# Performance work log

Hardware: AMD Instinct MI355X
Metric: run time of the kernel (lower is better)

## Reference

```python
import jax, jax.numpy as jnp
import numpy as np

D_ENC, D_DEC, HID = 512, 512, 256

def setup_inputs() -> dict:
    key = jax.random.key(0)
    ks = jax.random.split(key, 8)
    B, T, U = 4, 800, 150
    enc = jax.random.normal(ks[0], (B, T, D_ENC), dtype=jnp.float32)
    dec = jax.random.normal(ks[1], (B, U, D_DEC), dtype=jnp.float32)
    s_e = 1.0 / np.sqrt(D_ENC)
    s_d = 1.0 / np.sqrt(D_DEC)
    s_h = 1.0 / np.sqrt(HID)
    W_enc = jax.random.uniform(ks[2], (D_ENC, HID), jnp.float32, -s_e, s_e)
    b_enc = jax.random.uniform(ks[3], (HID,), jnp.float32, -s_e, s_e)
    W_dec = jax.random.uniform(ks[4], (D_DEC, HID), jnp.float32, -s_d, s_d)
    b_dec = jax.random.uniform(ks[5], (HID,), jnp.float32, -s_d, s_d)
    w_score = jax.random.uniform(ks[6], (HID,), jnp.float32, -s_h, s_h)
    b_score = jax.random.uniform(ks[7], (), jnp.float32, -s_h, s_h)
    return {"encoder_out": enc, "decoder_out": dec,
            "W_enc": W_enc, "b_enc": b_enc,
            "W_dec": W_dec, "b_dec": b_dec,
            "w_score": w_score, "b_score": b_score}

def reference(encoder_out, decoder_out, W_enc, b_enc, W_dec, b_dec, w_score, b_score):
    # enc_proj: [B,T,H], dec_proj: [B,U,H]
    enc_proj = jnp.einsum('bte,eh->bth', encoder_out, W_enc) + b_enc
    dec_proj = jnp.einsum('bud,dh->buh', decoder_out, W_dec) + b_dec
    # Broadcast-add + tanh -> [B,T,U,H], then reduce H with score vector.
    combined = jnp.tanh(enc_proj[:, :, None, :] + dec_proj[:, None, :, :])
    score = jnp.einsum('btuh,h->btu', combined, w_score) + b_score
    # Softmax over decoder tokens (last dim U).
    return jax.nn.softmax(score, axis=-1)
```

## Files before the change

kernel.cpp:

```cpp
#include <hip/hip_runtime.h>
#include <hip/hip_bf16.h>

#define B_ 4
#define T_ 800
#define U_ 150
#define D_ 512
#define H_ 256
#define PADH2 132

static constexpr float ARG_SCALE = 2.8853900817779268f;
static constexpr float LOG2E_F   = 1.4426950408889634f;

extern "C" __device__ float __ocml_exp2_f32(float);

__device__ __forceinline__ float fast_exp2(float x) {
#if __has_builtin(__builtin_amdgcn_exp2f)
    return __builtin_amdgcn_exp2f(x);
#else
    return __ocml_exp2_f32(x);
#endif
}
__device__ __forceinline__ float fast_rcp(float x) {
#if __has_builtin(__builtin_amdgcn_rcpf)
    return __builtin_amdgcn_rcpf(x);
#else
    return 1.0f / x;
#endif
}

__device__ __forceinline__ float4 fma4(float4 w, float x, float4 a) {
    a.x = fmaf(w.x, x, a.x); a.y = fmaf(w.y, x, a.y);
    a.z = fmaf(w.z, x, a.z); a.w = fmaf(w.w, x, a.w);
    return a;
}

__global__ __launch_bounds__(256) void proj_exp_kernel(
    const float* __restrict__ enc, const float* __restrict__ dec,
    const float* __restrict__ W_enc, const float* __restrict__ b_enc,
    const float* __restrict__ W_dec, const float* __restrict__ b_dec,
    float* __restrict__ Ee, float* __restrict__ Ed)
{
    const int tid = threadIdx.x;
    const int blk = blockIdx.x;
    const float* in; const float* Wm; const float* bias; float* outp; int row0;
    if (blk < 400) { in = enc; Wm = W_enc; bias = b_enc; outp = Ee; row0 = blk * 8; }
    else           { in = dec; Wm = W_dec; bias = b_dec; outp = Ed; row0 = (blk - 400) * 8; }

    const int h4  = tid & 63;
    const int wid = __builtin_amdgcn_readfirstlane(tid >> 6);
    const int eq  = wid * 128;

    const float* wp = Wm + (size_t)eq * H_ + 4 * h4;
    const float* ip0 = in + (size_t)(row0 + 0) * D_ + eq;
    const float* ip1 = in + (size_t)(row0 + 1) * D_ + eq;
    const float* ip2 = in + (size_t)(row0 + 2) * D_ + eq;
    const float* ip3 = in + (size_t)(row0 + 3) * D_ + eq;
    const float* ip4 = in + (size_t)(row0 + 4) * D_ + eq;
    const float* ip5 = in + (size_t)(row0 + 5) * D_ + eq;
    const float* ip6 = in + (size_t)(row0 + 6) * D_ + eq;
    const float* ip7 = in + (size_t)(row0 + 7) * D_ + eq;

    float4 acc[8] = {};
    #pragma unroll 2
    for (int e = 0; e < 128; e += 4) {
        float4 w0 = *(const float4*)(wp + (size_t)(e + 0) * H_);
        float4 w1 = *(const float4*)(wp + (size_t)(e + 1) * H_);
        float4 w2 = *(const float4*)(wp + (size_t)(e + 2) * H_);
        float4 w3 = *(const float4*)(wp + (size_t)(e + 3) * H_);
        float4 x0 = *(const float4*)(ip0 + e);
        float4 x1 = *(const float4*)(ip1 + e);
        float4 x2 = *(const float4*)(ip2 + e);
        float4 x3 = *(const float4*)(ip3 + e);
        float4 x4 = *(const float4*)(ip4 + e);
        float4 x5 = *(const float4*)(ip5 + e);
        float4 x6 = *(const float4*)(ip6 + e);
        float4 x7 = *(const float4*)(ip7 + e);
        acc[0] = fma4(w3, x0.w, fma4(w2, x0.z, fma4(w1, x0.y, fma4(w0, x0.x, acc[0]))));
        acc[1] = fma4(w3, x1.w, fma4(w2, x1.z, fma4(w1, x1.y, fma4(w0, x1.x, acc[1]))));
        acc[2] = fma4(w3, x2.w, fma4(w2, x2.z, fma4(w1, x2.y, fma4(w0, x2.x, acc[2]))));
        acc[3] = fma4(w3, x3.w, fma4(w2, x3.z, fma4(w1, x3.y, fma4(w0, x3.x, acc[3]))));
        acc[4] = fma4(w3, x4.w, fma4(w2, x4.z, fma4(w1, x4.y, fma4(w0, x4.x, acc[4]))));
        acc[5] = fma4(w3, x5.w, fma4(w2, x5.z, fma4(w1, x5.y, fma4(w0, x5.x, acc[5]))));
        acc[6] = fma4(w3, x6.w, fma4(w2, x6.z, fma4(w1, x6.y, fma4(w0, x6.x, acc[6]))));
        acc[7] = fma4(w3, x7.w, fma4(w2, x7.z, fma4(w1, x7.y, fma4(w0, x7.x, acc[7]))));
    }

    __shared__ float red[4][8][H_];
    #pragma unroll
    for (int r = 0; r < 8; ++r)
        *(float4*)&red[wid][r][4 * h4] = acc[r];
    __syncthreads();

    const int rr = tid >> 5;
    const int hq = tid & 31;
    #pragma unroll
    for (int s = 0; s < 2; ++s) {
        const int hp = hq + 32 * s;
        float4 a0 = *(const float4*)&red[0][rr][4 * hp];
        float4 a1 = *(const float4*)&red[1][rr][4 * hp];
        float4 a2 = *(const float4*)&red[2][rr][4 * hp];
        float4 a3 = *(const float4*)&red[3][rr][4 * hp];
        float4 b4 = *(const float4*)(bias + 4 * hp);
        float4 v;
        v.x = fast_exp2(ARG_SCALE * (((a0.x + a1.x) + (a2.x + a3.x)) + b4.x));
        v.y = fast_exp2(ARG_SCALE * (((a0.y + a1.y) + (a2.y + a3.y)) + b4.y));
        v.z = fast_exp2(ARG_SCALE * (((a0.z + a1.z) + (a2.z + a3.z)) + b4.z));
        v.w = fast_exp2(ARG_SCALE * (((a0.w + a1.w) + (a2.w + a3.w)) + b4.w));
        *(float4*)(outp + (size_t)(row0 + rr) * H_ + 4 * hp) = v;
    }
}

__global__ __launch_bounds__(128) void score_kernel(
    const float* __restrict__ Ee, const float* __restrict__ Ed,
    const float* __restrict__ w_score,
    float* __restrict__ sc0, float* __restrict__ sc1)
{
    const int tid = threadIdx.x;
    const int ut = blockIdx.x % 5, hs = blockIdx.x / 5;
    const int tt = blockIdx.y, b = blockIdx.z;

    __shared__ float eld[32][PADH2];
    __shared__ float dld[32][PADH2];

    const int t0 = tt * 32, u0 = ut * 32;
    const int hoff = hs * 128;

    #pragma unroll
    for (int k = 0; k < 8; ++k) {
        int idx = tid + 128 * k;
        int row = idx >> 5;
        int f4  = idx & 31;
        *(float4*)&eld[row][4 * f4] =
            *(const float4*)(Ee + (size_t)(b * T_ + t0 + row) * H_ + hoff + 4 * f4);
        int du = u0 + row; if (du > U_ - 1) du = U_ - 1;
        *(float4*)&dld[row][4 * f4] =
            *(const float4*)(Ed + (size_t)(b * U_ + du) * H_ + hoff + 4 * f4);
    }
    __syncthreads();

    const int tx = tid & 15, ty = tid >> 4;
    const float* e0 = &eld[4 * ty + 0][0];
    const float* e1 = &eld[4 * ty + 1][0];
    const float* e2 = &eld[4 * ty + 2][0];
    const float* e3 = &eld[4 * ty + 3][0];
    const float* d0 = &dld[tx][0];
    const float* d1 = &dld[tx + 16][0];
    const float* wp = w_score + hoff;

    float4 z4 = {0.f, 0.f, 0.f, 0.f};
    float4 a00 = z4, a01 = z4, a10 = z4, a11 = z4;
    float4 a20 = z4, a21 = z4, a30 = z4, a31 = z4;

#define SIG(E, D) fast_rcp(fmaf((E), (D), 1.f))
#define ROW(A, EV, DV) \
    A.x = fmaf(w.x, SIG(EV.x, DV.x), A.x); \
    A.y = fmaf(w.y, SIG(EV.y, DV.y), A.y); \
    A.z = fmaf(w.z, SIG(EV.z, DV.z), A.z); \
    A.w = fmaf(w.w, SIG(EV.w, DV.w), A.w);

    #pragma unroll 4
    for (int h4 = 0; h4 < 32; ++h4) {
        float4 w  = ((const float4*)wp)[h4];
        float4 ea = *(const float4*)(e0 + 4 * h4);
        float4 eb = *(const float4*)(e1 + 4 * h4);
        float4 ec = *(const float4*)(e2 + 4 * h4);
        float4 ed = *(const float4*)(e3 + 4 * h4);
        float4 da = *(const float4*)(d0 + 4 * h4);
        float4 db = *(const float4*)(d1 + 4 * h4);
        ROW(a00, ea, da) ROW(a01, ea, db)
        ROW(a10, eb, da) ROW(a11, eb, db)
        ROW(a20, ec, da) ROW(a21, ec, db)
        ROW(a30, ed, da) ROW(a31, ed, db)
    }
#undef ROW
#undef SIG

    float s0[4], s1[4];
    s0[0] = (a00.x + a00.y) + (a00.z + a00.w);
    s0[1] = (a10.x + a10.y) + (a10.z + a10.w);
    s0[2] = (a20.x + a20.y) + (a20.z + a20.w);
    s0[3] = (a30.x + a30.y) + (a30.z + a30.w);
    s1[0] = (a01.x + a01.y) + (a01.z + a01.w);
    s1[1] = (a11.x + a11.y) + (a11.z + a11.w);
    s1[2] = (a21.x + a21.y) + (a21.z + a21.w);
    s1[3] = (a31.x + a31.y) + (a31.z + a31.w);

    float* sout = hs ? sc1 : sc0;
    const int ua = u0 + tx, ub = ua + 16;
    #pragma unroll
    for (int j = 0; j < 4; ++j) {
        const int t = t0 + 4 * ty + j;
        const size_t base = (size_t)(b * T_ + t) * U_;
        sout[base + ua] = s0[j];
        if (ub < U_) sout[base + ub] = s1[j];
    }
}

__global__ __launch_bounds__(256) void softmax_kernel(
    const float* __restrict__ sc0, const float* __restrict__ sc1,
    float* __restrict__ out)
{
    const int tid  = threadIdx.x;
    const int wave = tid >> 6, lane = tid & 63;
    const int row  = blockIdx.x * 4 + wave;
    const size_t base = (size_t)row * U_;

    float z0 = -2.f * (sc0[base + lane]      + sc1[base + lane]);
    float z1 = -2.f * (sc0[base + lane + 64] + sc1[base + lane + 64]);
    const bool v2 = (lane + 128) < U_;
    float z2 = v2 ? -2.f * (sc0[base + lane + 128] + sc1[base + lane + 128])
                  : -INFINITY;

    float m = fmaxf(fmaxf(z0, z1), z2);
    #pragma unroll
    for (int off = 32; off > 0; off >>= 1) m = fmaxf(m, __shfl_xor(m, off));

    float p0 = fast_exp2((z0 - m) * LOG2E_F);
    float p1 = fast_exp2((z1 - m) * LOG2E_F);
    float p2 = v2 ? fast_exp2((z2 - m) * LOG2E_F) : 0.f;

    float s = p0 + p1 + p2;
    #pragma unroll
    for (int off = 32; off > 0; off >>= 1) s += __shfl_xor(s, off);

    const float inv = 1.0f / s;
    out[base + lane]      = p0 * inv;
    out[base + lane + 64] = p1 * inv;
    if (v2) out[base + lane + 128] = p2 * inv;
}

extern "C" void kernel_launch(void* const* d_in, const int* in_sizes, int n_in,
                              void* d_out, int out_size, void* d_ws, size_t ws_size,
                              hipStream_t stream) {
    const float* enc     = (const float*)d_in[0];
    const float* dec     = (const float*)d_in[1];
    const float* W_enc   = (const float*)d_in[2];
    const float* b_enc   = (const float*)d_in[3];
    const float* W_dec   = (const float*)d_in[4];
    const float* b_dec   = (const float*)d_in[5];
    const float* w_score = (const float*)d_in[6];

    float* ws = (float*)d_ws;
    float* Ee  = ws;
    float* Ed  = Ee + 819200;
    float* sc0 = Ed + 153600;
    float* sc1 = sc0 + 480000;
    float* out = (float*)d_out;

    proj_exp_kernel<<<475, 256, 0, stream>>>(enc, dec, W_enc, b_enc, W_dec, b_dec, Ee, Ed);
    score_kernel<<<dim3(10, 25, 4), 128, 0, stream>>>(Ee, Ed, w_score, sc0, sc1);
    softmax_kernel<<<800, 256, 0, stream>>>(sc0, sc1, out);
}
```

Before: 44.46 us.

## Move projection GEMMs to bf16x3 split MFMA with pre-swizzled weights

Replaces the FP32 FMA projection kernel with an MFMA kernel. It splits each fp32 value into bf16 hi and lo parts and uses three bf16 MFMAs to keep near-fp32 accuracy. A new per-call kernel converts and re-lays out the weights into the MFMA B-fragment order, and activations are staged through swizzled LDS. This targets the scalar-FMA cost of the projections, at the price of an extra kernel launch, the conversion traffic and a small loss of precision.

```diff
diff --git a/kernel.cpp b/kernel.cpp
--- a/kernel.cpp
+++ b/kernel.cpp
@@ -11,6 +11,9 @@
 static constexpr float ARG_SCALE = 2.8853900817779268f;
 static constexpr float LOG2E_F   = 1.4426950408889634f;
 
+typedef __attribute__((ext_vector_type(8))) short bf16x8;
+typedef __attribute__((ext_vector_type(4))) float f32x4;
+
 extern "C" __device__ float __ocml_exp2_f32(float);
 
 __device__ __forceinline__ float fast_exp2(float x) {
@@ -28,85 +31,114 @@
 #endif
 }
 
-__device__ __forceinline__ float4 fma4(float4 w, float x, float4 a) {
-    a.x = fmaf(w.x, x, a.x); a.y = fmaf(w.y, x, a.y);
-    a.z = fmaf(w.z, x, a.z); a.w = fmaf(w.w, x, a.w);
-    return a;
-}
-
-__global__ __launch_bounds__(256) void proj_exp_kernel(
+__device__ __forceinline__ void bf16split(float x, unsigned short& hi, unsigned short& lo) {
+    unsigned u = __builtin_bit_cast(unsigned, x);
+    unsigned r = (u + 0x7FFFu + ((u >> 16) & 1u)) >> 16;
+    hi = (unsigned short)r;
+    float fh = __builtin_bit_cast(float, r << 16);
+    float d = x - fh;
+    unsigned u2 = __builtin_bit_cast(unsigned, d);
+    unsigned r2 = (u2 + 0x7FFFu + ((u2 >> 16) & 1u)) >> 16;
+    lo = (unsigned short)r2;
+}
+
+__global__ __launch_bounds__(256) void wconv_kernel(
+    const float* __restrict__ We, const float* __restrict__ Wd,
+    unsigned short* __restrict__ WtEh, unsigned short* __restrict__ WtEl,
+    unsigned short* __restrict__ WtDh, unsigned short* __restrict__ WtDl)
+{
+    const int blk = blockIdx.x;
+    const float* W; unsigned short *oh, *ol; int e;
+    if (blk < 512) { W = We; oh = WtEh; ol = WtEl; e = blk; }
+    else           { W = Wd; oh = WtDh; ol = WtDl; e = blk - 512; }
+    const int h = threadIdx.x;
+    float x = W[(size_t)e * H_ + h];
+    unsigned short hi, lo; bf16split(x, hi, lo);
+    const int s = e >> 5, q = (e >> 3) & 3, j = e & 7;
+    const int g = h >> 4, r = h & 15, l = q * 16 + r;
+    const size_t idx = (size_t)(s * 16 + g) * 512 + l * 8 + j;
+    oh[idx] = hi; ol[idx] = lo;
+}
+
+__global__ __launch_bounds__(256) void proj_mfma_kernel(
     const float* __restrict__ enc, const float* __restrict__ dec,
-    const float* __restrict__ W_enc, const float* __restrict__ b_enc,
-    const float* __restrict__ W_dec, const float* __restrict__ b_dec,
+    const unsigned short* __restrict__ WtEh, const unsigned short* __restrict__ WtEl,
+    const unsigned short* __restrict__ WtDh, const unsigned short* __restrict__ WtDl,
+    const float* __restrict__ b_enc, const float* __restrict__ b_dec,
     float* __restrict__ Ee, float* __restrict__ Ed)
 {
     const int tid = threadIdx.x;
-    const int blk = blockIdx.x;
-    const float* in; const float* Wm; const float* bias; float* outp; int row0;
-    if (blk < 400) { in = enc; Wm = W_enc; bias = b_enc; outp = Ee; row0 = blk * 8; }
-    else           { in = dec; Wm = W_dec; bias = b_dec; outp = Ed; row0 = (blk - 400) * 8; }
-
-    const int h4  = tid & 63;
-    const int wid = __builtin_amdgcn_readfirstlane(tid >> 6);
-    const int eq  = wid * 128;
-
-    const float* wp = Wm + (size_t)eq * H_ + 4 * h4;
-    const float* ip0 = in + (size_t)(row0 + 0) * D_ + eq;
-    const float* ip1 = in + (size_t)(row0 + 1) * D_ + eq;
-    const float* ip2 = in + (size_t)(row0 + 2) * D_ + eq;
-    const float* ip3 = in + (size_t)(row0 + 3) * D_ + eq;
-    const float* ip4 = in + (size_t)(row0 + 4) * D_ + eq;
-    const float* ip5 = in + (size_t)(row0 + 5) * D_ + eq;
-    const float* ip6 = in + (size_t)(row0 + 6) * D_ + eq;
-    const float* ip7 = in + (size_t)(row0 + 7) * D_ + eq;
-
-    float4 acc[8] = {};
-    #pragma unroll 2
-    for (int e = 0; e < 128; e += 4) {
-        float4 w0 = *(const float4*)(wp + (size_t)(e + 0) * H_);
-        float4 w1 = *(const float4*)(wp + (size_t)(e + 1) * H_);
-        float4 w2 = *(const float4*)(wp + (size_t)(e + 2) * H_);
-        float4 w3 = *(const float4*)(wp + (size_t)(e + 3) * H_);
-        float4 x0 = *(const float4*)(ip0 + e);
-        float4 x1 = *(const float4*)(ip1 + e);
-        float4 x2 = *(const float4*)(ip2 + e);
-        float4 x3 = *(const float4*)(ip3 + e);
-        float4 x4 = *(const float4*)(ip4 + e);
-        float4 x5 = *(const float4*)(ip5 + e);
-        float4 x6 = *(const float4*)(ip6 + e);
-        float4 x7 = *(const float4*)(ip7 + e);
-        acc[0] = fma4(w3, x0.w, fma4(w2, x0.z, fma4(w1, x0.y, fma4(w0, x0.x, acc[0]))));
-        acc[1] = fma4(w3, x1.w, fma4(w2, x1.z, fma4(w1, x1.y, fma4(w0, x1.x, acc[1]))));
-        acc[2] = fma4(w3, x2.w, fma4(w2, x2.z, fma4(w1, x2.y, fma4(w0, x2.x, acc[2]))));
-        acc[3] = fma4(w3, x3.w, fma4(w2, x3.z, fma4(w1, x3.y, fma4(w0, x3.x, acc[3]))));
-        acc[4] = fma4(w3, x4.w, fma4(w2, x4.z, fma4(w1, x4.y, fma4(w0, x4.x, acc[4]))));
-        acc[5] = fma4(w3, x5.w, fma4(w2, x5.z, fma4(w1, x5.y, fma4(w0, x5.x, acc[5]))));
-        acc[6] = fma4(w3, x6.w, fma4(w2, x6.z, fma4(w1, x6.y, fma4(w0, x6.x, acc[6]))));
-        acc[7] = fma4(w3, x7.w, fma4(w2, x7.z, fma4(w1, x7.y, fma4(w0, x7.x, acc[7]))));
-    }
-
-    __shared__ float red[4][8][H_];
-    #pragma unroll
-    for (int r = 0; r < 8; ++r)
-        *(float4*)&red[wid][r][4 * h4] = acc[r];
+    int blk = blockIdx.x;
+    const float* in; const unsigned short *Wh, *Wl; const float* bias; float* outp;
+    int rmax;
+    if (blk < 400) { in = enc; Wh = WtEh; Wl = WtEl; bias = b_enc; outp = Ee; rmax = B_ * T_ - 1; }
+    else { blk -= 400; in = dec; Wh = WtDh; Wl = WtDl; bias = b_dec; outp = Ed; rmax = B_ * U_ - 1; }
+    const int hh   = blk & 1;
+    const int row0 = (blk >> 1) * 16;
+
+    __shared__ unsigned short Ah[16 * 512];
+    __shared__ unsigned short Al[16 * 512];
+
+    #pragma unroll
+    for (int k = 0; k < 4; ++k) {
+        const int chunk = tid + 256 * k;
+        const int r = chunk >> 6;
+        const int c = chunk & 63;
+        int gr = row0 + r; if (gr > rmax) gr = rmax;
+        const float* src = in + (size_t)gr * D_ + c * 8;
+        const float4 f0 = ((const float4*)src)[0];
+        const float4 f1 = ((const float4*)src)[1];
+        float v[8] = {f0.x, f0.y, f0.z, f0.w, f1.x, f1.y, f1.z, f1.w};
+        bf16x8 ah, al;
+        #pragma unroll
+        for (int j = 0; j < 8; ++j) {
+            unsigned short hi, lo; bf16split(v[j], hi, lo);
+            ah[j] = (short)hi; al[j] = (short)lo;
+        }
+        const int di = r * 512 + ((c ^ (r & 7)) << 3);
+        *(bf16x8*)&Ah[di] = ah;
+        *(bf16x8*)&Al[di] = al;
+    }
     __syncthreads();
 
-    const int rr = tid >> 5;
-    const int hq = tid & 31;
-    #pragma unroll
-    for (int s = 0; s < 2; ++s) {
-        const int hp = hq + 32 * s;
-        float4 a0 = *(const float4*)&red[0][rr][4 * hp];
-        float4 a1 = *(const float4*)&red[1][rr][4 * hp];
-        float4 a2 = *(const float4*)&red[2][rr][4 * hp];
-        float4 a3 = *(const float4*)&red[3][rr][4 * hp];
-        float4 b4 = *(const float4*)(bias + 4 * hp);
-        float4 v;
-        v.x = fast_exp2(ARG_SCALE * (((a0.x + a1.x) + (a2.x + a3.x)) + b4.x));
-        v.y = fast_exp2(ARG_SCALE * (((a0.y + a1.y) + (a2.y + a3.y)) + b4.y));
-        v.z = fast_exp2(ARG_SCALE * (((a0.z + a1.z) + (a2.z + a3.z)) + b4.z));
-        v.w = fast_exp2(ARG_SCALE * (((a0.w + a1.w) + (a2.w + a3.w)) + b4.w));
-        *(float4*)(outp + (size_t)(row0 + rr) * H_ + 4 * hp) = v;
+    const int lane = tid & 63, w = tid >> 6;
+    const int q = lane >> 4, r15 = lane & 15;
+
+    f32x4 acc0 = {0.f, 0.f, 0.f, 0.f};
+    f32x4 acc1 = {0.f, 0.f, 0.f, 0.f};
+
+    const unsigned short* bh0 = Wh + (size_t)(8 * hh + 2 * w) * 512 + lane * 8;
+    const unsigned short* bl0 = Wl + (size_t)(8 * hh + 2 * w) * 512 + lane * 8;
+
+    #pragma unroll 4
+    for (int s = 0; s < 16; ++s) {
+        const int ai = r15 * 512 + ((((s << 2) + q) ^ (r15 & 7)) << 3);
+        const bf16x8 ahf = *(const bf16x8*)&Ah[ai];
+        const bf16x8 alf = *(const bf16x8*)&Al[ai];
+        const size_t so = (size_t)(s * 16) * 512;
+        const bf16x8 bh_0 = *(const bf16x8*)(bh0 + so);
+        const bf16x8 bl_0 = *(const bf16x8*)(bl0 + so);
+        const bf16x8 bh_1 = *(const bf16x8*)(bh0 + so + 512);
+        const bf16x8 bl_1 = *(const bf16x8*)(bl0 + so + 512);
+        acc0 = __builtin_amdgcn_mfma_f32_16x16x32_bf16(ahf, bh_0, acc0, 0, 0, 0);
+        acc0 = __builtin_amdgcn_mfma_f32_16x16x32_bf16(ahf, bl_0, acc0, 0, 0, 0);
+        acc0 = __builtin_amdgcn_mfma_f32_16x16x32_bf16(alf, bh_0, acc0, 0, 0, 0);
+        acc1 = __builtin_amdgcn_mfma_f32_16x16x32_bf16(ahf, bh_1, acc1, 0, 0, 0);
+        acc1 = __builtin_amdgcn_mfma_f32_16x16x32_bf16(ahf, bl_1, acc1, 0, 0, 0);
+        acc1 = __builtin_amdgcn_mfma_f32_16x16x32_bf16(alf, bh_1, acc1, 0, 0, 0);
+    }
+
+    #pragma unroll
+    for (int nt = 0; nt < 2; ++nt) {
+        const int h = 128 * hh + 32 * w + nt * 16 + r15;
+        const float bv = bias[h];
+        const f32x4 a = nt ? acc1 : acc0;
+        #pragma unroll
+        for (int reg = 0; reg < 4; ++reg) {
+            const int trow = row0 + 4 * q + reg;
+            if (trow <= rmax)
+                outp[(size_t)trow * H_ + h] = fast_exp2(ARG_SCALE * (a[reg] + bv));
+        }
     }
 }
 
@@ -245,9 +277,15 @@
     float* Ed  = Ee + 819200;
     float* sc0 = Ed + 153600;
     float* sc1 = sc0 + 480000;
+    unsigned short* WtEh = (unsigned short*)(sc1 + 480000);
+    unsigned short* WtEl = WtEh + 131072;
+    unsigned short* WtDh = WtEl + 131072;
+    unsigned short* WtDl = WtDh + 131072;
     float* out = (float*)d_out;
 
-    proj_exp_kernel<<<475, 256, 0, stream>>>(enc, dec, W_enc, b_enc, W_dec, b_dec, Ee, Ed);
+    wconv_kernel<<<1024, 256, 0, stream>>>(W_enc, W_dec, WtEh, WtEl, WtDh, WtDl);
+    proj_mfma_kernel<<<476, 256, 0, stream>>>(enc, dec, WtEh, WtEl, WtDh, WtDl,
+                                              b_enc, b_dec, Ee, Ed);
     score_kernel<<<dim3(10, 25, 4), 128, 0, stream>>>(Ee, Ed, w_score, sc0, sc1);
     softmax_kernel<<<800, 256, 0, stream>>>(sc0, sc1, out);
 }
```

New measurement: 44.51 us. No clear change (+0.1%).
